# Kernel tuning notes

Measured on AMD Instinct MI355X. Metric: run time of the kernel, lower is better.

## Reference

```python
import jax, jax.numpy as jnp
import numpy as np

N_NODES = 100000
N_EDGES = 320000
DIM = 128
BN_EPS = 1e-5
AGG_EPS = 1e-6


def setup_inputs() -> dict:
    key = jax.random.key(0)
    ks = jax.random.split(key, 12)
    s = 1.0 / np.sqrt(DIM)
    inp = {
        "x": jax.random.normal(ks[0], (N_NODES, DIM), dtype=jnp.float32),
        "e": jax.random.normal(ks[1], (N_EDGES, DIM), dtype=jnp.float32),
        "edge_index": jax.random.randint(ks[2], (2, N_EDGES), 0, N_NODES, dtype=jnp.int32),
        "Wa": jax.random.normal(ks[3], (DIM, DIM), dtype=jnp.float32) * s,
        "ba": jnp.zeros((DIM,), dtype=jnp.float32),
        "Wb": jax.random.normal(ks[4], (DIM, DIM), dtype=jnp.float32) * s,
        "bb": jnp.zeros((DIM,), dtype=jnp.float32),
        "Wd": jax.random.normal(ks[5], (DIM, DIM), dtype=jnp.float32) * s,
        "bd": jnp.zeros((DIM,), dtype=jnp.float32),
        "We": jax.random.normal(ks[6], (DIM, DIM), dtype=jnp.float32) * s,
        "be": jnp.zeros((DIM,), dtype=jnp.float32),
        "gamma": jnp.ones((DIM,), dtype=jnp.float32),
        "beta": jnp.zeros((DIM,), dtype=jnp.float32),
    }
    return inp


def reference(x, e, edge_index, Wa, ba, Wb, bb, Wd, bd, We, be, gamma, beta):
    # PyG source_to_target flow: j = edge_index[0] (source), i = edge_index[1] (target)
    src = edge_index[0]
    dst = edge_index[1]

    Ax = x @ Wa + ba
    Bx = x @ Wb + bb
    Dx = x @ Wd + bd
    Ex = x @ We + be

    # message: e_ij = Dx_i + Ex_j ; sigma = sigmoid(e_ij)  [n_edges, out_dim]
    e_ij = Dx[dst] + Ex[src]
    sigma = jax.nn.sigmoid(e_ij)

    # aggregate: gated mean over incoming edges of each target node
    num = jax.ops.segment_sum(sigma * Bx[src], dst, num_segments=N_NODES)
    den = jax.ops.segment_sum(sigma, dst, num_segments=N_NODES)
    aggr = num / (den + AGG_EPS)

    # update + BatchNorm (training stats, biased var) + ReLU; dropout=0, residual=False
    h = Ax + aggr
    mean = jnp.mean(h, axis=0)
    var = jnp.mean(jnp.square(h - mean), axis=0)
    h_norm = (h - mean) * jax.lax.rsqrt(var + BN_EPS)
    x_out = jax.nn.relu(gamma * h_norm + beta)

    # edge output is raw e_ij (bn_edge_e is never applied in forward)
    return x_out, e_ij
```

## Files before the change

kernel.cpp:

```cpp
#include <hip/hip_runtime.h>
#include <hip/hip_bf16.h>
#include <stdint.h>

#define N_NODES 100000
#define N_EDGES 320000
#define DIM 128
#define AGG_EPS 1e-6f
#define BN_EPS 1e-5f
#define NODE_BLOCKS 2048
#define SCAN_BLOCKS 391

typedef float f32x4 __attribute__((ext_vector_type(4)));
typedef __bf16 bf16x8 __attribute__((ext_vector_type(8)));

__device__ __forceinline__ uint32_t f2bf(float f) {
  union { float f; uint32_t u; } v; v.f = f;
  uint32_t u = v.u;
  return (u + 0x7fffu + ((u >> 16) & 1u)) >> 16;
}
__device__ __forceinline__ float bf2f(uint32_t h) {
  union { uint32_t u; float f; } v; v.u = h << 16;
  return v.f;
}


__global__ __launch_bounds__(256) void k_prep(
    const float* __restrict__ Wa, const float* __restrict__ ba,
    const float* __restrict__ Wb, const float* __restrict__ bb,
    const float* __restrict__ Wd, const float* __restrict__ bd,
    const float* __restrict__ We, const float* __restrict__ be,
    ushort* __restrict__ wt, float* __restrict__ biasc,
    uint4* __restrict__ cnt_zero) {
  __shared__ float tile[64][65];
  const int tid = threadIdx.x;
  const int b = blockIdx.x;
  const int sel = b >> 2, tr = (b >> 1) & 1, tc = b & 1;
  const float* W = (sel == 0) ? Wa : (sel == 1) ? Wb : (sel == 2) ? Wd : We;
#pragma unroll
  for (int i = 0; i < 16; ++i) {
    int idx = tid + 256 * i;
    int lr = idx >> 6, lc = idx & 63;
    tile[lr][lc] = W[(tr * 64 + lr) * 128 + tc * 64 + lc];
  }
  __syncthreads();
#pragma unroll
  for (int i = 0; i < 16; ++i) {
    int idx = tid + 256 * i;
    int oc = idx >> 6, ok = idx & 63;
    wt[(sel * 128 + tc * 64 + oc) * 128 + tr * 64 + ok] = (ushort)f2bf(tile[ok][oc]);
  }
  if (b == 0) {
    for (int t = tid; t < 512; t += 256) {
      int s2 = t >> 7;
      const float* bp = (s2 == 0) ? ba : (s2 == 1) ? bb : (s2 == 2) ? bd : be;
      biasc[t] = bp[t & 127];
    }
  }
  for (int j = b * 256 + tid; j < 25000; j += 16 * 256)
    cnt_zero[j] = make_uint4(0u, 0u, 0u, 0u);
}

__global__ __launch_bounds__(256) void k_gemm(
    const float* __restrict__ x, const ushort* __restrict__ wt,
    const float* __restrict__ biasc, ushort* __restrict__ abde) {
  __shared__ ushort As[64 * 128];
  __shared__ ushort Bs[64 * 128];
  const int tid = threadIdx.x;
  const int m0 = blockIdx.x * 64;

#pragma unroll
  for (int i = 0; i < 4; ++i) {
    int qid = tid + 256 * i;
    int row = qid >> 4, q = qid & 15;
    int gr = m0 + row;
    uint4 pk = make_uint4(0u, 0u, 0u, 0u);
    if (gr < N_NODES) {
      const float* s = x + (size_t)gr * 128 + q * 8;
      float4 f0 = *(const float4*)(s);
      float4 f1 = *(const float4*)(s + 4);
      pk.x = f2bf(f0.x) | (f2bf(f0.y) << 16);
      pk.y = f2bf(f0.z) | (f2bf(f0.w) << 16);
      pk.z = f2bf(f1.x) | (f2bf(f1.y) << 16);
      pk.w = f2bf(f1.z) | (f2bf(f1.w) << 16);
    }
    int byte = (row * 256 + q * 16) ^ ((row & 7) << 4);
    *(uint4*)((char*)As + byte) = pk;
  }
  __syncthreads();

  const int w = tid >> 6, lane = tid & 63;
  const int r = lane & 15, g = lane >> 4;
  const int arow = w * 16 + r;

  bf16x8 afrag[4];
#pragma unroll
  for (int kk = 0; kk < 4; ++kk) {
    int ab = (arow * 256 + kk * 64 + g * 16) ^ ((arow & 7) << 4);
    afrag[kk] = *(const bf16x8*)((const char*)As + ab);
  }

  const int ntpair[4][2] = {{2, 6}, {3, 7}, {0, 4}, {1, 5}};
  for (int ph = 0; ph < 4; ++ph) {
    f32x4 acc[2][4] = {};
#pragma unroll
    for (int t2 = 0; t2 < 2; ++t2) {
      if (ph | t2) __syncthreads();
      const int n0 = ntpair[ph][t2] * 64;
#pragma unroll
      for (int i = 0; i < 4; ++i) {
        int qid = tid + 256 * i;
        int row = qid >> 4, q = qid & 15;
        uint4 v = *(const uint4*)(wt + (n0 + row) * 128 + q * 8);
        int byte = (row * 256 + q * 16) ^ ((row & 7) << 4);
        *(uint4*)((char*)Bs + byte) = v;
      }
      __syncthreads();
#pragma unroll
      for (int kk = 0; kk < 4; ++kk) {
#pragma unroll
        for (int n = 0; n < 4; ++n) {
          int brow = n * 16 + r;
          int bb = (brow * 256 + kk * 64 + g * 16) ^ ((brow & 7) << 4);
          bf16x8 bv = *(const bf16x8*)((const char*)Bs + bb);
          acc[t2][n] = __builtin_amdgcn_mfma_f32_16x16x32_bf16(afrag[kk], bv, acc[t2][n], 0, 0, 0);
        }
      }
    }
#pragma unroll
    for (int t2 = 0; t2 < 2; ++t2) {
      float bias = biasc[ntpair[ph][t2] * 64 + 0 * 16 + r];
#pragma unroll
      for (int n = 0; n < 4; ++n) {
        int lc = t2 * 64 + n * 16 + r;
        float bsv = biasc[ntpair[ph][t2] * 64 + n * 16 + r];
#pragma unroll
        for (int q = 0; q < 4; ++q) {
          int row = w * 16 + g * 4 + q;
          As[row * 128 + (lc ^ (((row >> 2) & 3) << 4))] = (ushort)f2bf(acc[t2][n][q] + bsv);
        }
      }
      (void)bias;
    }
    __syncthreads();
#pragma unroll
    for (int it = 0; it < 4; ++it) {
      int u = tid + 256 * it;
      int row = u >> 4, mq = u & 15;
      int xo = ((row >> 2) & 3) << 4;
      uint2 lo = *(const uint2*)&As[row * 128 + ((4 * mq) ^ xo)];
      uint2 hi = *(const uint2*)&As[row * 128 + ((64 + 4 * mq) ^ xo)];
      uint4 val = (ph < 2) ? make_uint4(hi.x, lo.x, hi.y, lo.y)
                           : make_uint4(lo.x, hi.x, lo.y, hi.y);
      int gr = m0 + row;
      if (gr < N_NODES)
        *(uint4*)((char*)abde + (size_t)gr * 1024 + (ph * 16 + mq) * 16) = val;
    }
  }
}

__global__ __launch_bounds__(256) void k_count(const int* __restrict__ dst,
                                               int* __restrict__ cnt) {
  int t = blockIdx.x * 256 + threadIdx.x;
  if (t < N_EDGES) atomicAdd(&cnt[dst[t]], 1);
}

__global__ __launch_bounds__(256) void k_bsum(const int* __restrict__ cnt,
                                              int* __restrict__ bsum) {
  __shared__ int lds[256];
  int t = threadIdx.x;
  int i = blockIdx.x * 256 + t;
  lds[t] = (i < N_NODES) ? cnt[i] : 0;
  __syncthreads();
#pragma unroll
  for (int off = 128; off > 0; off >>= 1) {
    if (t < off) lds[t] += lds[t + off];
    __syncthreads();
  }
  if (t == 0) bsum[blockIdx.x] = lds[0];
}

__global__ __launch_bounds__(512) void k_scanb(const int* __restrict__ bsum,
                                               int* __restrict__ boff,
                                               int* __restrict__ row_ptr) {
  __shared__ int lds[512];
  int t = threadIdx.x;
  int v = (t < SCAN_BLOCKS) ? bsum[t] : 0;
  lds[t] = v;
  __syncthreads();
  for (int off = 1; off < 512; off <<= 1) {
    int u = (t >= off) ? lds[t - off] : 0;
    __syncthreads();
    lds[t] += u;
    __syncthreads();
  }
  if (t < SCAN_BLOCKS) boff[t] = lds[t] - v;
  if (t == SCAN_BLOCKS - 1) row_ptr[N_NODES] = lds[t];
}

__global__ __launch_bounds__(256) void k_scan3(const int* __restrict__ cnt,
                                               const int* __restrict__ boff,
                                               int* __restrict__ row_ptr,
                                               int* __restrict__ cursor) {
  __shared__ int lds[256];
  int t = threadIdx.x;
  int i = blockIdx.x * 256 + t;
  int v = (i < N_NODES) ? cnt[i] : 0;
  lds[t] = v;
  __syncthreads();
  for (int off = 1; off < 256; off <<= 1) {
    int u = (t >= off) ? lds[t - off] : 0;
    __syncthreads();
    lds[t] += u;
    __syncthreads();
  }
  if (i < N_NODES) {
    int ex = boff[blockIdx.x] + lds[t] - v;
    row_ptr[i] = ex;
    cursor[i] = ex;
  }
}

__global__ __launch_bounds__(256) void k_scatter(const int* __restrict__ dst,
                                                 int* __restrict__ cursor,
                                                 int* __restrict__ csr_eid) {
  int t = blockIdx.x * 256 + threadIdx.x;
  if (t < N_EDGES) {
    int d = dst[t];
    int pos = atomicAdd(&cursor[d], 1);
    csr_eid[pos] = t;
  }
}

__global__ __launch_bounds__(256) void k_node(
    const ushort* __restrict__ abde, const int* __restrict__ row_ptr,
    const int* __restrict__ csr_eid, const int* __restrict__ esrc,
    float* __restrict__ out_e, ushort* __restrict__ h,
    float* __restrict__ partials) {
  const int tid = threadIdx.x;
  const int lane = tid & 63;
  const int wid = (blockIdx.x << 2) | (tid >> 6);
  const int nw = NODE_BLOCKS * 4;
  float s0 = 0.f, s1 = 0.f, q0 = 0.f, q1 = 0.f;

  int i = wid;
  int k0 = 0, ke = 0;
  uint2 ad = make_uint2(0u, 0u);
  if (i < N_NODES) {
    k0 = row_ptr[i];
    ke = row_ptr[i + 1];
    ad = *(const uint2*)((const char*)abde + (size_t)i * 1024 + 512 + lane * 8);
  }
  while (i < N_NODES) {
    const int inext = i + nw;
    int nk0 = 0, nke = 0;
    uint2 nad = make_uint2(0u, 0u);
    if (inext < N_NODES) {
      nk0 = row_ptr[inext];
      nke = row_ptr[inext + 1];
      nad = *(const uint2*)((const char*)abde + (size_t)inext * 1024 + 512 + lane * 8);
    }
    float ax0 = bf2f(ad.x & 0xffffu), ax1 = bf2f(ad.x >> 16);
    float dx0 = bf2f(ad.y & 0xffffu), dx1 = bf2f(ad.y >> 16);
    float n0 = 0.f, n1 = 0.f, d0 = 0.f, d1 = 0.f;
    for (int base = k0; base < ke; base += 64) {
      const int cnt = min(64, ke - base);
      int eidv = 0, srcv = 0;
      if (lane < cnt) {
        eidv = csr_eid[base + lane];
        srcv = esrc[eidv];
      }
      int j = 0;
      for (; j + 2 <= cnt; j += 2) {
        int eA = __shfl(eidv, j),     sA = __shfl(srcv, j);
        int eB = __shfl(eidv, j + 1), sB = __shfl(srcv, j + 1);
        uint2 ebA = *(const uint2*)((const char*)abde + (size_t)sA * 1024 + lane * 8);
        uint2 ebB = *(const uint2*)((const char*)abde + (size_t)sB * 1024 + lane * 8);
        float e0 = dx0 + bf2f(ebA.x & 0xffffu);
        float e1 = dx1 + bf2f(ebA.x >> 16);
        *(float2*)(out_e + (size_t)eA * 128 + 2 * lane) = make_float2(e0, e1);
        float sg0 = 1.f / (1.f + __expf(-e0));
        float sg1 = 1.f / (1.f + __expf(-e1));
        n0 += sg0 * bf2f(ebA.y & 0xffffu);
        n1 += sg1 * bf2f(ebA.y >> 16);
        d0 += sg0; d1 += sg1;
        float f0 = dx0 + bf2f(ebB.x & 0xffffu);
        float f1 = dx1 + bf2f(ebB.x >> 16);
        *(float2*)(out_e + (size_t)eB * 128 + 2 * lane) = make_float2(f0, f1);
        float tg0 = 1.f / (1.f + __expf(-f0));
        float tg1 = 1.f / (1.f + __expf(-f1));
        n0 += tg0 * bf2f(ebB.y & 0xffffu);
        n1 += tg1 * bf2f(ebB.y >> 16);
        d0 += tg0; d1 += tg1;
      }
      if (j < cnt) {
        int eA = __shfl(eidv, j), sA = __shfl(srcv, j);
        uint2 ebA = *(const uint2*)((const char*)abde + (size_t)sA * 1024 + lane * 8);
        float e0 = dx0 + bf2f(ebA.x & 0xffffu);
        float e1 = dx1 + bf2f(ebA.x >> 16);
        *(float2*)(out_e + (size_t)eA * 128 + 2 * lane) = make_float2(e0, e1);
        float sg0 = 1.f / (1.f + __expf(-e0));
        float sg1 = 1.f / (1.f + __expf(-e1));
        n0 += sg0 * bf2f(ebA.y & 0xffffu);
        n1 += sg1 * bf2f(ebA.y >> 16);
        d0 += sg0; d1 += sg1;
      }
    }
    float h0 = ax0 + n0 / (d0 + AGG_EPS);
    float h1 = ax1 + n1 / (d1 + AGG_EPS);
    *(uint32_t*)(h + (size_t)i * 128 + 2 * lane) = f2bf(h0) | (f2bf(h1) << 16);
    s0 += h0; s1 += h1; q0 += h0 * h0; q1 += h1 * h1;
    i = inext; k0 = nk0; ke = nke; ad = nad;
  }
  __shared__ float red[256 * 4];
  red[tid] = s0; red[256 + tid] = s1; red[512 + tid] = q0; red[768 + tid] = q1;
  __syncthreads();
  if (tid < 64) {
    float vs0 = red[tid] + red[tid + 64] + red[tid + 128] + red[tid + 192];
    float vs1 = red[256 + tid] + red[256 + tid + 64] + red[256 + tid + 128] + red[256 + tid + 192];
    float vq0 = red[512 + tid] + red[512 + tid + 64] + red[512 + tid + 128] + red[512 + tid + 192];
    float vq1 = red[768 + tid] + red[768 + tid + 64] + red[768 + tid + 128] + red[768 + tid + 192];
    float* p = partials + blockIdx.x * 256;
    p[2 * tid] = vs0;
    p[2 * tid + 1] = vs1;
    p[128 + 2 * tid] = vq0;
    p[128 + 2 * tid + 1] = vq1;
  }
}

__global__ __launch_bounds__(256) void k_stats1(const float* __restrict__ partials,
                                                float* __restrict__ out2) {
  int t = threadIdx.x, b = blockIdx.x;
  float s = 0.f;
#pragma unroll
  for (int j = 0; j < 32; ++j) s += partials[(b * 32 + j) * 256 + t];
  out2[b * 256 + t] = s;
}

__global__ __launch_bounds__(128) void k_stats2(const float* __restrict__ out2,
                                                float* __restrict__ stats) {
  int c = threadIdx.x;
  float s = 0.f, q = 0.f;
#pragma unroll
  for (int b = 0; b < 64; ++b) {
    s += out2[b * 256 + c];
    q += out2[b * 256 + 128 + c];
  }
  float mean = s * (1.f / (float)N_NODES);
  float var = q * (1.f / (float)N_NODES) - mean * mean;
  stats[c] = mean;
  stats[128 + c] = rsqrtf(var + BN_EPS);
}

__global__ __launch_bounds__(256) void k_final(const ushort* __restrict__ h,
    const float* __restrict__ gamma, const float* __restrict__ beta,
    const float* __restrict__ stats, float* __restrict__ out_x) {
  int idx = blockIdx.x * 256 + threadIdx.x;
  int c = (idx & 15) * 8;
  uint4 hv = *(const uint4*)(h + idx * 8);
  uint32_t hw[4] = {hv.x, hv.y, hv.z, hv.w};
  float out[8];
#pragma unroll
  for (int j = 0; j < 8; ++j) {
    uint32_t u = (j & 1) ? (hw[j >> 1] >> 16) : (hw[j >> 1] & 0xffffu);
    float hf = bf2f(u);
    int cc = c + j;
    float v = gamma[cc] * (hf - stats[cc]) * stats[128 + cc] + beta[cc];
    out[j] = fmaxf(v, 0.f);
  }
  *(float4*)(out_x + idx * 8) = make_float4(out[0], out[1], out[2], out[3]);
  *(float4*)(out_x + idx * 8 + 4) = make_float4(out[4], out[5], out[6], out[7]);
}

extern "C" void kernel_launch(void* const* d_in, const int* in_sizes, int n_in,
                              void* d_out, int out_size, void* d_ws, size_t ws_size,
                              hipStream_t stream) {
  const float* x = (const float*)d_in[0];
  const int* edge_index = (const int*)d_in[2];
  const float* Wa = (const float*)d_in[3];
  const float* ba = (const float*)d_in[4];
  const float* Wb = (const float*)d_in[5];
  const float* bb = (const float*)d_in[6];
  const float* Wd = (const float*)d_in[7];
  const float* bd = (const float*)d_in[8];
  const float* We = (const float*)d_in[9];
  const float* be = (const float*)d_in[10];
  const float* gamma = (const float*)d_in[11];
  const float* beta = (const float*)d_in[12];

  const int* src = edge_index;
  const int* dst = edge_index + N_EDGES;

  char* w = (char*)d_ws;
  ushort* wt      = (ushort*)(w);
  float*  biasc   = (float*)(w + 131072);
  ushort* abde    = (ushort*)(w + 133120);
  ushort* hbuf    = (ushort*)(w + 102533120);
  int*    cnt     = (int*)(w + 128133120);
  int*    row_ptr = (int*)(w + 128533120);
  int*    cursor  = (int*)(w + 128933248);
  int*    csr_eid = (int*)(w + 129333248);
  float*  partials= (float*)(w + 130613248);
  float*  stats   = (float*)(w + 132710400);

  int*   bsum = (int*)partials;
  int*   boff = (int*)(partials + 512);
  float* out2 = (float*)cnt;

  float* out_x = (float*)d_out;
  float* out_e = out_x + (size_t)N_NODES * DIM;

  k_prep<<<16, 256, 0, stream>>>(Wa, ba, Wb, bb, Wd, bd, We, be, wt, biasc, (uint4*)cnt);
  k_gemm<<<1563, 256, 0, stream>>>(x, wt, biasc, abde);
  k_count<<<(N_EDGES + 255) / 256, 256, 0, stream>>>(dst, cnt);
  k_bsum<<<SCAN_BLOCKS, 256, 0, stream>>>(cnt, bsum);
  k_scanb<<<1, 512, 0, stream>>>(bsum, boff, row_ptr);
  k_scan3<<<SCAN_BLOCKS, 256, 0, stream>>>(cnt, boff, row_ptr, cursor);
  k_scatter<<<(N_EDGES + 255) / 256, 256, 0, stream>>>(dst, cursor, csr_eid);
  k_node<<<NODE_BLOCKS, 256, 0, stream>>>(abde, row_ptr, csr_eid, src, out_e, hbuf, partials);
  k_stats1<<<64, 256, 0, stream>>>(partials, out2);
  k_stats2<<<1, 128, 0, stream>>>(out2, stats);
  k_final<<<6250, 256, 0, stream>>>(hbuf, gamma, beta, stats, out_x);
}
```

Measured before the change: 200.8 us.

## Merge CSR scan kernels, store src in CSR order, unroll edge loop by four

The count kernel now also accumulates per-256-node bucket sums with atomics, so the separate block-sum and block-scan kernels are replaced by a single scan kernel that computes each block's offset locally. The scatter kernel writes source indices in CSR order into scratch space aliased on the output buffer, removing a dependent gather inside the node kernel. The node kernel's per-edge loop is unrolled by four so more row gathers are in flight at once. This cuts two kernel launches and one indirection, at the cost of extra atomics and more register pressure.

```diff
diff --git a/kernel.cpp b/kernel.cpp
--- a/kernel.cpp
+++ b/kernel.cpp
@@ -30,7 +30,7 @@
     const float* __restrict__ Wd, const float* __restrict__ bd,
     const float* __restrict__ We, const float* __restrict__ be,
     ushort* __restrict__ wt, float* __restrict__ biasc,
-    uint4* __restrict__ cnt_zero) {
+    uint4* __restrict__ cnt_zero, uint4* __restrict__ bsum2_zero) {
   __shared__ float tile[64][65];
   const int tid = threadIdx.x;
   const int b = blockIdx.x;
@@ -58,6 +58,7 @@
   }
   for (int j = b * 256 + tid; j < 25000; j += 16 * 256)
     cnt_zero[j] = make_uint4(0u, 0u, 0u, 0u);
+  if (b == 0 && tid < 100) bsum2_zero[tid] = make_uint4(0u, 0u, 0u, 0u);
 }
 
 __global__ __launch_bounds__(256) void k_gemm(
@@ -128,7 +129,6 @@
     }
 #pragma unroll
     for (int t2 = 0; t2 < 2; ++t2) {
-      float bias = biasc[ntpair[ph][t2] * 64 + 0 * 16 + r];
 #pragma unroll
       for (int n = 0; n < 4; ++n) {
         int lc = t2 * 64 + n * 16 + r;
@@ -139,7 +139,6 @@
           As[row * 128 + (lc ^ (((row >> 2) & 3) << 4))] = (ushort)f2bf(acc[t2][n][q] + bsv);
         }
       }
-      (void)bias;
     }
     __syncthreads();
 #pragma unroll
@@ -159,50 +158,40 @@
 }
 
 __global__ __launch_bounds__(256) void k_count(const int* __restrict__ dst,
-                                               int* __restrict__ cnt) {
+                                               int* __restrict__ cnt,
+                                               int* __restrict__ bsum2) {
   int t = blockIdx.x * 256 + threadIdx.x;
-  if (t < N_EDGES) atomicAdd(&cnt[dst[t]], 1);
-}
-
-__global__ __launch_bounds__(256) void k_bsum(const int* __restrict__ cnt,
-                                              int* __restrict__ bsum) {
+  if (t < N_EDGES) {
+    int d = dst[t];
+    atomicAdd(&cnt[d], 1);
+    atomicAdd(&bsum2[d >> 8], 1);
+  }
+}
+
+__global__ __launch_bounds__(256) void k_scan(const int* __restrict__ cnt,
+                                              const int* __restrict__ bsum2,
+                                              int* __restrict__ row_ptr,
+                                              int* __restrict__ cursor) {
+  __shared__ int ps[256];
   __shared__ int lds[256];
-  int t = threadIdx.x;
-  int i = blockIdx.x * 256 + t;
-  lds[t] = (i < N_NODES) ? cnt[i] : 0;
+  __shared__ int boff_s;
+  const int t = threadIdx.x;
+  int a = (2 * t < SCAN_BLOCKS) ? bsum2[2 * t] : 0;
+  int b = (2 * t + 1 < SCAN_BLOCKS) ? bsum2[2 * t + 1] : 0;
+  ps[t] = a + b;
   __syncthreads();
-#pragma unroll
-  for (int off = 128; off > 0; off >>= 1) {
-    if (t < off) lds[t] += lds[t + off];
+  for (int off = 1; off < 256; off <<= 1) {
+    int v = (t >= off) ? ps[t - off] : 0;
     __syncthreads();
-  }
-  if (t == 0) bsum[blockIdx.x] = lds[0];
-}
-
-__global__ __launch_bounds__(512) void k_scanb(const int* __restrict__ bsum,
-                                               int* __restrict__ boff,
-                                               int* __restrict__ row_ptr) {
-  __shared__ int lds[512];
-  int t = threadIdx.x;
-  int v = (t < SCAN_BLOCKS) ? bsum[t] : 0;
-  lds[t] = v;
-  __syncthreads();
-  for (int off = 1; off < 512; off <<= 1) {
-    int u = (t >= off) ? lds[t - off] : 0;
+    ps[t] += v;
     __syncthreads();
-    lds[t] += u;
-    __syncthreads();
-  }
-  if (t < SCAN_BLOCKS) boff[t] = lds[t] - v;
-  if (t == SCAN_BLOCKS - 1) row_ptr[N_NODES] = lds[t];
-}
-
-__global__ __launch_bounds__(256) void k_scan3(const int* __restrict__ cnt,
-                                               const int* __restrict__ boff,
-                                               int* __restrict__ row_ptr,
-                                               int* __restrict__ cursor) {
-  __shared__ int lds[256];
-  int t = threadIdx.x;
+  }
+  if (t == 0) {
+    int b0 = blockIdx.x, p = b0 >> 1;
+    int pre = (p > 0) ? ps[p - 1] : 0;
+    if (b0 & 1) pre += bsum2[b0 - 1];
+    boff_s = pre;
+  }
   int i = blockIdx.x * 256 + t;
   int v = (i < N_NODES) ? cnt[i] : 0;
   lds[t] = v;
@@ -214,26 +203,31 @@
     __syncthreads();
   }
   if (i < N_NODES) {
-    int ex = boff[blockIdx.x] + lds[t] - v;
+    int ex = boff_s + lds[t] - v;
     row_ptr[i] = ex;
     cursor[i] = ex;
   }
+  if (blockIdx.x == 0 && t == 0) row_ptr[N_NODES] = N_EDGES;
 }
 
 __global__ __launch_bounds__(256) void k_scatter(const int* __restrict__ dst,
+                                                 const int* __restrict__ srcArr,
                                                  int* __restrict__ cursor,
-                                                 int* __restrict__ csr_eid) {
+                                                 int* __restrict__ csr_eid,
+                                                 int* __restrict__ csr_src) {
   int t = blockIdx.x * 256 + threadIdx.x;
   if (t < N_EDGES) {
     int d = dst[t];
+    int s = srcArr[t];
     int pos = atomicAdd(&cursor[d], 1);
     csr_eid[pos] = t;
+    csr_src[pos] = s;
   }
 }
 
 __global__ __launch_bounds__(256) void k_node(
     const ushort* __restrict__ abde, const int* __restrict__ row_ptr,
-    const int* __restrict__ csr_eid, const int* __restrict__ esrc,
+    const int* __restrict__ csr_eid, const int* __restrict__ csr_src,
     float* __restrict__ out_e, ushort* __restrict__ h,
     float* __restrict__ partials) {
   const int tid = threadIdx.x;
@@ -267,9 +261,40 @@
       int eidv = 0, srcv = 0;
       if (lane < cnt) {
         eidv = csr_eid[base + lane];
-        srcv = esrc[eidv];
+        srcv = csr_src[base + lane];
       }
       int j = 0;
+      for (; j + 4 <= cnt; j += 4) {
+        int eA = __shfl(eidv, j),     sA = __shfl(srcv, j);
+        int eB = __shfl(eidv, j + 1), sB = __shfl(srcv, j + 1);
+        int eC = __shfl(eidv, j + 2), sC = __shfl(srcv, j + 2);
+        int eD = __shfl(eidv, j + 3), sD = __shfl(srcv, j + 3);
+        uint2 ebA = *(const uint2*)((const char*)abde + (size_t)sA * 1024 + lane * 8);
+        uint2 ebB = *(const uint2*)((const char*)abde + (size_t)sB * 1024 + lane * 8);
+        uint2 ebC = *(const uint2*)((const char*)abde + (size_t)sC * 1024 + lane * 8);
+        uint2 ebD = *(const uint2*)((const char*)abde + (size_t)sD * 1024 + lane * 8);
+        float e0, e1, sg0, sg1;
+        e0 = dx0 + bf2f(ebA.x & 0xffffu); e1 = dx1 + bf2f(ebA.x >> 16);
+        *(float2*)(out_e + (size_t)eA * 128 + 2 * lane) = make_float2(e0, e1);
+        sg0 = 1.f / (1.f + __expf(-e0)); sg1 = 1.f / (1.f + __expf(-e1));
+        n0 += sg0 * bf2f(ebA.y & 0xffffu); n1 += sg1 * bf2f(ebA.y >> 16);
+        d0 += sg0; d1 += sg1;
+        e0 = dx0 + bf2f(ebB.x & 0xffffu); e1 = dx1 + bf2f(ebB.x >> 16);
+        *(float2*)(out_e + (size_t)eB * 128 + 2 * lane) = make_float2(e0, e1);
+        sg0 = 1.f / (1.f + __expf(-e0)); sg1 = 1.f / (1.f + __expf(-e1));
+        n0 += sg0 * bf2f(ebB.y & 0xffffu); n1 += sg1 * bf2f(ebB.y >> 16);
+        d0 += sg0; d1 += sg1;
+        e0 = dx0 + bf2f(ebC.x & 0xffffu); e1 = dx1 + bf2f(ebC.x >> 16);
+        *(float2*)(out_e + (size_t)eC * 128 + 2 * lane) = make_float2(e0, e1);
+        sg0 = 1.f / (1.f + __expf(-e0)); sg1 = 1.f / (1.f + __expf(-e1));
+        n0 += sg0 * bf2f(ebC.y & 0xffffu); n1 += sg1 * bf2f(ebC.y >> 16);
+        d0 += sg0; d1 += sg1;
+        e0 = dx0 + bf2f(ebD.x & 0xffffu); e1 = dx1 + bf2f(ebD.x >> 16);
+        *(float2*)(out_e + (size_t)eD * 128 + 2 * lane) = make_float2(e0, e1);
+        sg0 = 1.f / (1.f + __expf(-e0)); sg1 = 1.f / (1.f + __expf(-e1));
+        n0 += sg0 * bf2f(ebD.y & 0xffffu); n1 += sg1 * bf2f(ebD.y >> 16);
+        d0 += sg0; d1 += sg1;
+      }
       for (; j + 2 <= cnt; j += 2) {
         int eA = __shfl(eidv, j),     sA = __shfl(srcv, j);
         int eB = __shfl(eidv, j + 1), sB = __shfl(srcv, j + 1);
@@ -280,16 +305,14 @@
         *(float2*)(out_e + (size_t)eA * 128 + 2 * lane) = make_float2(e0, e1);
         float sg0 = 1.f / (1.f + __expf(-e0));
         float sg1 = 1.f / (1.f + __expf(-e1));
-        n0 += sg0 * bf2f(ebA.y & 0xffffu);
-        n1 += sg1 * bf2f(ebA.y >> 16);
+        n0 += sg0 * bf2f(ebA.y & 0xffffu); n1 += sg1 * bf2f(ebA.y >> 16);
         d0 += sg0; d1 += sg1;
         float f0 = dx0 + bf2f(ebB.x & 0xffffu);
         float f1 = dx1 + bf2f(ebB.x >> 16);
         *(float2*)(out_e + (size_t)eB * 128 + 2 * lane) = make_float2(f0, f1);
         float tg0 = 1.f / (1.f + __expf(-f0));
         float tg1 = 1.f / (1.f + __expf(-f1));
-        n0 += tg0 * bf2f(ebB.y & 0xffffu);
-        n1 += tg1 * bf2f(ebB.y >> 16);
+        n0 += tg0 * bf2f(ebB.y & 0xffffu); n1 += tg1 * bf2f(ebB.y >> 16);
         d0 += tg0; d1 += tg1;
       }
       if (j < cnt) {
@@ -300,8 +323,7 @@
         *(float2*)(out_e + (size_t)eA * 128 + 2 * lane) = make_float2(e0, e1);
         float sg0 = 1.f / (1.f + __expf(-e0));
         float sg1 = 1.f / (1.f + __expf(-e1));
-        n0 += sg0 * bf2f(ebA.y & 0xffffu);
-        n1 += sg1 * bf2f(ebA.y >> 16);
+        n0 += sg0 * bf2f(ebA.y & 0xffffu); n1 += sg1 * bf2f(ebA.y >> 16);
         d0 += sg0; d1 += sg1;
       }
     }
@@ -402,21 +424,20 @@
   float*  partials= (float*)(w + 130613248);
   float*  stats   = (float*)(w + 132710400);
 
-  int*   bsum = (int*)partials;
-  int*   boff = (int*)(partials + 512);
-  float* out2 = (float*)cnt;
+  int*   bsum2 = (int*)partials;
+  float* out2  = (float*)cnt;
 
   float* out_x = (float*)d_out;
   float* out_e = out_x + (size_t)N_NODES * DIM;
-
-  k_prep<<<16, 256, 0, stream>>>(Wa, ba, Wb, bb, Wd, bd, We, be, wt, biasc, (uint4*)cnt);
+  int* csr_src = (int*)out_x;
+
+  k_prep<<<16, 256, 0, stream>>>(Wa, ba, Wb, bb, Wd, bd, We, be, wt, biasc,
+                                 (uint4*)cnt, (uint4*)bsum2);
   k_gemm<<<1563, 256, 0, stream>>>(x, wt, biasc, abde);
-  k_count<<<(N_EDGES + 255) / 256, 256, 0, stream>>>(dst, cnt);
-  k_bsum<<<SCAN_BLOCKS, 256, 0, stream>>>(cnt, bsum);
-  k_scanb<<<1, 512, 0, stream>>>(bsum, boff, row_ptr);
-  k_scan3<<<SCAN_BLOCKS, 256, 0, stream>>>(cnt, boff, row_ptr, cursor);
-  k_scatter<<<(N_EDGES + 255) / 256, 256, 0, stream>>>(dst, cursor, csr_eid);
-  k_node<<<NODE_BLOCKS, 256, 0, stream>>>(abde, row_ptr, csr_eid, src, out_e, hbuf, partials);
+  k_count<<<(N_EDGES + 255) / 256, 256, 0, stream>>>(dst, cnt, bsum2);
+  k_scan<<<SCAN_BLOCKS, 256, 0, stream>>>(cnt, bsum2, row_ptr, cursor);
+  k_scatter<<<(N_EDGES + 255) / 256, 256, 0, stream>>>(dst, src, cursor, csr_eid, csr_src);
+  k_node<<<NODE_BLOCKS, 256, 0, stream>>>(abde, row_ptr, csr_eid, csr_src, out_e, hbuf, partials);
   k_stats1<<<64, 256, 0, stream>>>(partials, out2);
   k_stats2<<<1, 128, 0, stream>>>(out2, stats);
   k_final<<<6250, 256, 0, stream>>>(hbuf, gamma, beta, stats, out_x);
```

Result: slower. 309.5 us (+54.2%).
